# Performance work log

Hardware: AMD Instinct MI355X
Metric: run time of the kernel (lower is better)

The kernel has to match this reference:

```python
import jax, jax.numpy as jnp
import numpy as np
import math

B, S, HID = 1, 2048, 4096
NH, NKV, HD = 32, 8, 128
ROPE_THETA = 500000.0
NEG = -1e9

def _rope_tables(seq_len, head_dim, theta):
    inv_freq = 1.0 / (theta ** (np.arange(0, head_dim, 2, dtype=np.float32) / head_dim))
    t = np.arange(seq_len, dtype=np.float32)
    freqs = np.outer(t, inv_freq)                      # [S, HD/2]
    emb = np.concatenate([freqs, freqs], axis=-1)      # [S, HD]
    return jnp.asarray(np.cos(emb))[None], jnp.asarray(np.sin(emb))[None]  # [1,S,HD]

def setup_inputs() -> dict:
    key = jax.random.key(0)
    ks = jax.random.split(key, 6)
    hidden_states = jax.random.normal(ks[0], (B, S, HID), jnp.float32)
    # causal additive mask [B,1,S,S]
    causal = jnp.triu(jnp.full((S, S), NEG, jnp.float32), k=1)
    attention_mask = jnp.broadcast_to(causal, (B, 1, S, S))
    cos, sin = _rope_tables(S, HD, ROPE_THETA)
    sc = 0.02
    wq = jax.random.normal(ks[1], (NH * HD, HID), jnp.float32) * sc
    wk = jax.random.normal(ks[2], (NKV * HD, HID), jnp.float32) * sc
    wv = jax.random.normal(ks[3], (NKV * HD, HID), jnp.float32) * sc
    wo = jax.random.normal(ks[4], (HID, NH * HD), jnp.float32) * sc
    return {"hidden_states": hidden_states, "attention_mask": attention_mask,
            "cos": cos, "sin": sin, "wq": wq, "wk": wk, "wv": wv, "wo": wo}

def _rotate_half(x):
    x1, x2 = jnp.split(x, 2, axis=-1)
    return jnp.concatenate([-x2, x1], axis=-1)

def reference(hidden_states, attention_mask, cos, sin, wq, wk, wv, wo):
    b, s, _ = hidden_states.shape
    # QKV projections (torch Linear: x @ W^T)
    q = jnp.einsum('bsm,nm->bsn', hidden_states, wq).reshape(b, s, NH, HD).transpose(0, 2, 1, 3)
    k = jnp.einsum('bsm,nm->bsn', hidden_states, wk).reshape(b, s, NKV, HD).transpose(0, 2, 1, 3)
    v = jnp.einsum('bsm,nm->bsn', hidden_states, wv).reshape(b, s, NKV, HD).transpose(0, 2, 1, 3)
    # RoPE (cos/sin broadcast over heads via unsqueeze dim 1)
    c = cos[:, None, :, :]
    sn = sin[:, None, :, :]
    q = q * c + _rotate_half(q) * sn
    k = k * c + _rotate_half(k) * sn
    # GQA: repeat kv heads
    n_rep = NH // NKV
    k = jnp.repeat(k, n_rep, axis=1)
    v = jnp.repeat(v, n_rep, axis=1)
    scores = jnp.einsum('bhqd,bhkd->bhqk', q, k) / math.sqrt(HD)
    scores = scores + attention_mask[:, :, :, :s]
    attn = jax.nn.softmax(scores.astype(jnp.float32), axis=-1).astype(q.dtype)
    out = jnp.einsum('bhqk,bhkd->bhqd', attn, v)        # [b,NH,s,HD]
    out = out.transpose(0, 2, 1, 3).reshape(b, s, NH * HD)
    return jnp.einsum('bsn,mn->bsm', out, wo)
```

## Files before the change

### kernel.cpp

```cpp
#include <hip/hip_runtime.h>
#include <hip/hip_bf16.h>
#include <stdint.h>

typedef __hip_bfloat16 bf16;
using bf16x8 = __attribute__((ext_vector_type(8))) short;
using f32x4  = __attribute__((ext_vector_type(4))) float;

#define MFMA16(a, b, c) __builtin_amdgcn_mfma_f32_16x16x32_bf16(a, b, c, 0, 0, 0)

#define S_LEN 2048
#define HID   4096
#define NH    32
#define NKV   8
#define HD    128
#define DQ    4096
#define DKV   1024
#define QK_SCALE 0.1275228868824805f

__device__ inline void gl_lds16(const bf16* g, bf16* l) {
    __builtin_amdgcn_global_load_lds(
        (const __attribute__((address_space(1))) void*)g,
        (__attribute__((address_space(3))) void*)l, 16, 0, 0);
}

__device__ inline void cvt_store4(const float* src, bf16* dst, size_t i4) {
    float4 v = ((const float4*)src)[i4];
    union { ushort4 u; bf16 h[4]; } pk;
    pk.h[0] = __float2bfloat16(v.x);
    pk.h[1] = __float2bfloat16(v.y);
    pk.h[2] = __float2bfloat16(v.z);
    pk.h[3] = __float2bfloat16(v.w);
    ((ushort4*)dst)[i4] = pk.u;
}

__global__ void conv_all(const float* __restrict__ hidden, const float* __restrict__ wq,
                         const float* __restrict__ wk, const float* __restrict__ wv,
                         bf16* __restrict__ hb, bf16* __restrict__ wqd,
                         bf16* __restrict__ wkd, bf16* __restrict__ wvd) {
    const size_t M1 = 1024 * 1024;
#pragma unroll
    for (int j = 0; j < 4; ++j) {
        size_t idx = (size_t)blockIdx.x * 1024 + j * 256 + threadIdx.x;
        if (idx < 2 * M1)      cvt_store4(hidden, hb,  idx);
        else if (idx < 6 * M1) cvt_store4(wq,     wqd, idx - 2 * M1);
        else if (idx < 7 * M1) cvt_store4(wk,     wkd, idx - 6 * M1);
        else                   cvt_store4(wv,     wvd, idx - 7 * M1);
    }
}

__global__ void conv_wo(const float* __restrict__ wo, bf16* __restrict__ wod) {
#pragma unroll
    for (int j = 0; j < 4; ++j) {
        size_t idx = (size_t)blockIdx.x * 1024 + j * 256 + threadIdx.x;
        cvt_store4(wo, wod, idx);
    }
}

__global__ void __launch_bounds__(256, 2)
qkv_gemm(const bf16* __restrict__ A, const bf16* __restrict__ Bq,
         const bf16* __restrict__ Bk, const bf16* __restrict__ Bv,
         bf16* __restrict__ Cq, bf16* __restrict__ Ck, bf16* __restrict__ Cv) {
    __shared__ __align__(16) bf16 As[128][64];
    __shared__ __align__(16) bf16 Bs[128][64];

    const int bx = blockIdx.x;
    int mode, bn;
    const bf16* B;
    if (bx < 32)      { mode = 0; B = Bq; bn = bx * 128; }
    else if (bx < 40) { mode = 1; B = Bk; bn = (bx - 32) * 128; }
    else              { mode = 2; B = Bv; bn = (bx - 40) * 128; }

    const int tid  = threadIdx.x;
    const int bm   = blockIdx.y * 128;
    const int wave = tid >> 6, lane = tid & 63;
    const int quad = lane >> 4, l15 = lane & 15;
    const int wr   = (wave >> 1) * 64;
    const int wc   = (wave & 1) * 64;

    f32x4 acc[4][4] = {};

    for (int k0 = 0; k0 < HID; k0 += 64) {
#pragma unroll
        for (int i = 0; i < 4; ++i) {
            int idx = tid + i * 256;
            int r   = idx >> 3;
            int c   = (idx & 7) * 8;
            gl_lds16(&A[(size_t)(bm + r) * HID + k0 + c], &As[r][c]);
            gl_lds16(&B[(size_t)(bn + r) * HID + k0 + c], &Bs[r][c]);
        }
        __syncthreads();
#pragma unroll
        for (int kk = 0; kk < 64; kk += 32) {
            bf16x8 a[4], b[4];
#pragma unroll
            for (int i = 0; i < 4; ++i)
                a[i] = *(const bf16x8*)(&As[wr + i * 16 + l15][kk + quad * 8]);
#pragma unroll
            for (int i = 0; i < 4; ++i)
                b[i] = *(const bf16x8*)(&Bs[wc + i * 16 + l15][kk + quad * 8]);
#pragma unroll
            for (int mi = 0; mi < 4; ++mi)
#pragma unroll
                for (int ni = 0; ni < 4; ++ni)
                    acc[mi][ni] = MFMA16(a[mi], b[ni], acc[mi][ni]);
        }
        __syncthreads();
    }

    if (mode == 0) {
#pragma unroll
        for (int mi = 0; mi < 4; ++mi)
#pragma unroll
            for (int ni = 0; ni < 4; ++ni)
#pragma unroll
                for (int r = 0; r < 4; ++r)
                    Cq[(size_t)(bm + wr + mi * 16 + quad * 4 + r) * DQ +
                       bn + wc + ni * 16 + l15] = __float2bfloat16(acc[mi][ni][r]);
    } else if (mode == 1) {
#pragma unroll
        for (int mi = 0; mi < 4; ++mi)
#pragma unroll
            for (int ni = 0; ni < 4; ++ni)
#pragma unroll
                for (int r = 0; r < 4; ++r)
                    Ck[(size_t)(bm + wr + mi * 16 + quad * 4 + r) * DKV +
                       bn + wc + ni * 16 + l15] = __float2bfloat16(acc[mi][ni][r]);
    } else {
#pragma unroll
        for (int mi = 0; mi < 4; ++mi)
#pragma unroll
            for (int ni = 0; ni < 4; ++ni) {
                int row0 = bm + wr + mi * 16 + quad * 4;
                int col  = bn + wc + ni * 16 + l15;
                union { ushort4 u; bf16 h[4]; } pk;
#pragma unroll
                for (int r = 0; r < 4; ++r) pk.h[r] = __float2bfloat16(acc[mi][ni][r]);
                *(ushort4*)(&Cv[(size_t)col * S_LEN + row0]) = pk.u;
            }
    }
}

__global__ void __launch_bounds__(256, 2)
out_gemm(const bf16* __restrict__ A, const bf16* __restrict__ B,
         float* __restrict__ C) {
    __shared__ __align__(16) bf16 As[128][64];
    __shared__ __align__(16) bf16 Bs[128][64];

    const int tid  = threadIdx.x;
    const int bm   = blockIdx.y * 128;
    const int bn   = blockIdx.x * 128;
    const int wave = tid >> 6, lane = tid & 63;
    const int quad = lane >> 4, l15 = lane & 15;
    const int wr   = (wave >> 1) * 64;
    const int wc   = (wave & 1) * 64;

    f32x4 acc[4][4] = {};

    for (int k0 = 0; k0 < DQ; k0 += 64) {
#pragma unroll
        for (int i = 0; i < 4; ++i) {
            int idx = tid + i * 256;
            int r   = idx >> 3;
            int c   = (idx & 7) * 8;
            gl_lds16(&A[(size_t)(bm + r) * DQ + k0 + c], &As[r][c]);
            gl_lds16(&B[(size_t)(bn + r) * DQ + k0 + c], &Bs[r][c]);
        }
        __syncthreads();
#pragma unroll
        for (int kk = 0; kk < 64; kk += 32) {
            bf16x8 a[4], b[4];
#pragma unroll
            for (int i = 0; i < 4; ++i)
                a[i] = *(const bf16x8*)(&As[wr + i * 16 + l15][kk + quad * 8]);
#pragma unroll
            for (int i = 0; i < 4; ++i)
                b[i] = *(const bf16x8*)(&Bs[wc + i * 16 + l15][kk + quad * 8]);
#pragma unroll
            for (int mi = 0; mi < 4; ++mi)
#pragma unroll
                for (int ni = 0; ni < 4; ++ni)
                    acc[mi][ni] = MFMA16(a[mi], b[ni], acc[mi][ni]);
        }
        __syncthreads();
    }

#pragma unroll
    for (int mi = 0; mi < 4; ++mi)
#pragma unroll
        for (int ni = 0; ni < 4; ++ni)
#pragma unroll
            for (int r = 0; r < 4; ++r)
                C[(size_t)(bm + wr + mi * 16 + quad * 4 + r) * HID +
                  bn + wc + ni * 16 + l15] = acc[mi][ni][r];
}

__global__ void rope_all(bf16* __restrict__ q, bf16* __restrict__ k,
                         const float* __restrict__ cosb, const float* __restrict__ sinb) {
    int idx = blockIdx.x * 256 + threadIdx.x;
    const int nq = S_LEN * NH * 64;
    bf16* x;
    int nheads;
    float mul;
    if (idx < nq) { x = q; nheads = NH; mul = QK_SCALE; }
    else          { x = k; nheads = NKV; mul = 1.0f; idx -= nq; }
    int d = idx & 63;
    int h = (idx >> 6) % nheads;
    int s = idx / (nheads * 64);
    size_t base = (size_t)s * nheads * 128 + (size_t)h * 128 + d;
    float x1 = __bfloat162float(x[base]);
    float x2 = __bfloat162float(x[base + 64]);
    x[base]      = __float2bfloat16((x1 * cosb[s * 128 + d]      - x2 * sinb[s * 128 + d])      * mul);
    x[base + 64] = __float2bfloat16((x2 * cosb[s * 128 + d + 64] + x1 * sinb[s * 128 + d + 64]) * mul);
}

__device__ __forceinline__ void stage_kv(const bf16* __restrict__ Kp,
                                         const bf16* __restrict__ Vp,
                                         bf16* ks, bf16* vs, int t0, int tid) {
#pragma unroll
    for (int i = 0; i < 4; ++i) {
        int idx = tid + i * 256;
        int t   = idx >> 4;
        int c8  = ((idx & 15) - t) & 15;
        gl_lds16(&Kp[(size_t)(t0 + t) * DKV + c8 * 8], &ks[idx * 8]);
        int d   = idx >> 3;
        int tc  = ((idx & 7) - d) & 7;
        gl_lds16(&Vp[(size_t)d * S_LEN + t0 + tc * 8], &vs[idx * 8]);
    }
}

__global__ void __launch_bounds__(256, 2)
flash_attn(const bf16* Q, const bf16* __restrict__ K,
           const bf16* __restrict__ Vt, bf16* O) {
    __shared__ __align__(16) bf16 Ks[2][64 * 128];
    __shared__ __align__(16) bf16 Vs[2][128 * 64];
    __shared__ __align__(16) bf16 p_lds[4][16][72];

    const int xb   = (int)gridDim.x - 1 - (int)blockIdx.x;
    const int head = blockIdx.y;
    const int kvh  = head >> 2;
    const int tid  = threadIdx.x;
    const int wave = tid >> 6, lane = tid & 63;
    const int quad = lane >> 4, l15 = lane & 15;
    const int q0w  = xb * 64 + wave * 16;

    const bf16* Kp = K + kvh * HD;
    const bf16* Vp = Vt + (size_t)kvh * HD * S_LEN;

    bf16x8 qf[4];
#pragma unroll
    for (int c = 0; c < 4; ++c)
        qf[c] = *(const bf16x8*)(&Q[(size_t)(q0w + l15) * DQ + head * HD + c * 32 + quad * 8]);

    f32x4 o_acc[8] = {};
    float l_part[4] = {0.f, 0.f, 0.f, 0.f};

    const int t_max = (xb + 1) * 64;

    stage_kv(Kp, Vp, &Ks[0][0], &Vs[0][0], 0, tid);
    asm volatile("s_waitcnt vmcnt(0)" ::: "memory");
    __builtin_amdgcn_sched_barrier(0);
    __builtin_amdgcn_s_barrier();
    __builtin_amdgcn_sched_barrier(0);

    int cur = 0;
    for (int t0 = 0; t0 < t_max; t0 += 64) {
        if (t0 + 64 < t_max)
            stage_kv(Kp, Vp, &Ks[cur ^ 1][0], &Vs[cur ^ 1][0], t0 + 64, tid);
        __builtin_amdgcn_sched_barrier(0);

        const bf16* ksb = &Ks[cur][0];
        const bf16* vsb = &Vs[cur][0];

        f32x4 sc[4] = {};
        __builtin_amdgcn_s_setprio(1);
#pragma unroll
        for (int h = 0; h < 4; ++h) {
            int t = h * 16 + l15;
#pragma unroll
            for (int c = 0; c < 4; ++c) {
                bf16x8 kf = *(const bf16x8*)(&ksb[t * 128 + ((c * 4 + quad + t) & 15) * 8]);
                sc[h] = MFMA16(qf[c], kf, sc[h]);
            }
        }
        __builtin_amdgcn_s_setprio(0);

        if (t0 + 64 > q0w) {
#pragma unroll
            for (int r = 0; r < 4; ++r) {
                const int q = q0w + quad * 4 + r;
                float lsum = 0.f;
#pragma unroll
                for (int h = 0; h < 4; ++h) {
                    float a = (t0 + h * 16 + l15 > q) ? -1e30f : sc[h][r];
                    float p = exp2f(a);
                    lsum += p;
                    p_lds[wave][quad * 4 + r][h * 16 + l15] = __float2bfloat16(p);
                }
                l_part[r] += lsum;
            }
        } else {
#pragma unroll
            for (int r = 0; r < 4; ++r) {
                float lsum = 0.f;
#pragma unroll
                for (int h = 0; h < 4; ++h) {
                    float p = exp2f(sc[h][r]);
                    lsum += p;
                    p_lds[wave][quad * 4 + r][h * 16 + l15] = __float2bfloat16(p);
                }
                l_part[r] += lsum;
            }
        }

        asm volatile("" ::: "memory");
        bf16x8 pf0 = *(const bf16x8*)(&p_lds[wave][l15][quad * 8]);
        bf16x8 pf1 = *(const bf16x8*)(&p_lds[wave][l15][32 + quad * 8]);
        __builtin_amdgcn_s_setprio(1);
#pragma unroll
        for (int db = 0; db < 8; ++db) {
            int d = db * 16 + l15;
            bf16x8 vf0 = *(const bf16x8*)(&vsb[d * 64 + ((quad + d) & 7) * 8]);
            bf16x8 vf1 = *(const bf16x8*)(&vsb[d * 64 + ((4 + quad + d) & 7) * 8]);
            o_acc[db] = MFMA16(pf0, vf0, o_acc[db]);
            o_acc[db] = MFMA16(pf1, vf1, o_acc[db]);
        }
        __builtin_amdgcn_s_setprio(0);

        __builtin_amdgcn_sched_barrier(0);
        asm volatile("s_waitcnt vmcnt(0)" ::: "memory");
        __builtin_amdgcn_sched_barrier(0);
        __builtin_amdgcn_s_barrier();
        __builtin_amdgcn_sched_barrier(0);
        cur ^= 1;
    }

#pragma unroll
    for (int r = 0; r < 4; ++r) {
        float l = l_part[r];
        l += __shfl_xor(l, 1);
        l += __shfl_xor(l, 2);
        l += __shfl_xor(l, 4);
        l += __shfl_xor(l, 8);
        float inv = 1.0f / l;
        int row = q0w + quad * 4 + r;
#pragma unroll
        for (int db = 0; db < 8; ++db)
            O[(size_t)row * DQ + head * HD + db * 16 + l15] =
                __float2bfloat16(o_acc[db][r] * inv);
    }
}

extern "C" void kernel_launch(void* const* d_in, const int* in_sizes, int n_in,
                              void* d_out, int out_size, void* d_ws, size_t ws_size,
                              hipStream_t stream) {
    const float* hidden = (const float*)d_in[0];
    const float* cosb   = (const float*)d_in[2];
    const float* sinb   = (const float*)d_in[3];
    const float* wq     = (const float*)d_in[4];
    const float* wk     = (const float*)d_in[5];
    const float* wv     = (const float*)d_in[6];
    const float* wo     = (const float*)d_in[7];
    float* out = (float*)d_out;

    const size_t M1 = 1024 * 1024;
    bf16* hb  = (bf16*)d_ws;
    bf16* wkd = hb + 8 * M1;
    bf16* wvd = hb + 12 * M1;
    bf16* wod = hb;
    bf16* qb  = hb + 16 * M1;
    bf16* kb  = hb + 24 * M1;
    bf16* vt  = hb + 26 * M1;
    bf16* wqd = (bf16*)d_out;

    conv_all<<<8192, 256, 0, stream>>>(hidden, wq, wk, wv, hb, wqd, wkd, wvd);
    qkv_gemm<<<dim3(48, 16), 256, 0, stream>>>(hb, wqd, wkd, wvd, qb, kb, vt);
    conv_wo<<<4096, 256, 0, stream>>>(wo, wod);
    rope_all<<<(S_LEN * (NH + NKV) * 64) / 256, 256, 0, stream>>>(qb, kb, cosb, sinb);
    flash_attn<<<dim3(32, 32), 256, 0, stream>>>(qb, kb, vt, qb);
    out_gemm<<<dim3(32, 16), 256, 0, stream>>>(qb, wod, out);
}
```

Baseline: 561.1 us.

## Swizzle GEMM LDS tiles, vectorize RoPE, load V directly to registers in attention

Both GEMMs now store A/B tiles in LDS with an XOR-style rotation of 16-byte slots per row, so the MFMA fragment reads avoid bank conflicts. RoPE processes four elements per thread with vector loads of the bf16 data and the cos/sin tables, cutting thread count and scalar memory ops. Flash attention drops the V LDS staging and reads V fragments from global memory straight into registers, which frees LDS so the launch bound can target three blocks per SM. The direct V loads are not double-buffered and may expose global latency and raise register pressure.

```diff
diff --git a/kernel.cpp b/kernel.cpp
--- a/kernel.cpp
+++ b/kernel.cpp
@@ -82,22 +82,27 @@
     for (int k0 = 0; k0 < HID; k0 += 64) {
 #pragma unroll
         for (int i = 0; i < 4; ++i) {
-            int idx = tid + i * 256;
-            int r   = idx >> 3;
-            int c   = (idx & 7) * 8;
-            gl_lds16(&A[(size_t)(bm + r) * HID + k0 + c], &As[r][c]);
-            gl_lds16(&B[(size_t)(bn + r) * HID + k0 + c], &Bs[r][c]);
+            int idx  = tid + i * 256;
+            int r    = idx >> 3;
+            int slot = idx & 7;
+            int c    = ((slot - r) & 7) * 8;
+            gl_lds16(&A[(size_t)(bm + r) * HID + k0 + c], &As[r][slot * 8]);
+            gl_lds16(&B[(size_t)(bn + r) * HID + k0 + c], &Bs[r][slot * 8]);
         }
         __syncthreads();
 #pragma unroll
         for (int kk = 0; kk < 64; kk += 32) {
             bf16x8 a[4], b[4];
 #pragma unroll
-            for (int i = 0; i < 4; ++i)
-                a[i] = *(const bf16x8*)(&As[wr + i * 16 + l15][kk + quad * 8]);
-#pragma unroll
-            for (int i = 0; i < 4; ++i)
-                b[i] = *(const bf16x8*)(&Bs[wc + i * 16 + l15][kk + quad * 8]);
+            for (int i = 0; i < 4; ++i) {
+                int row = wr + i * 16 + l15;
+                a[i] = *(const bf16x8*)(&As[row][(((kk >> 3) + quad + row) & 7) * 8]);
+            }
+#pragma unroll
+            for (int i = 0; i < 4; ++i) {
+                int row = wc + i * 16 + l15;
+                b[i] = *(const bf16x8*)(&Bs[row][(((kk >> 3) + quad + row) & 7) * 8]);
+            }
 #pragma unroll
             for (int mi = 0; mi < 4; ++mi)
 #pragma unroll
@@ -159,22 +164,27 @@
     for (int k0 = 0; k0 < DQ; k0 += 64) {
 #pragma unroll
         for (int i = 0; i < 4; ++i) {
-            int idx = tid + i * 256;
-            int r   = idx >> 3;
-            int c   = (idx & 7) * 8;
-            gl_lds16(&A[(size_t)(bm + r) * DQ + k0 + c], &As[r][c]);
-            gl_lds16(&B[(size_t)(bn + r) * DQ + k0 + c], &Bs[r][c]);
+            int idx  = tid + i * 256;
+            int r    = idx >> 3;
+            int slot = idx & 7;
+            int c    = ((slot - r) & 7) * 8;
+            gl_lds16(&A[(size_t)(bm + r) * DQ + k0 + c], &As[r][slot * 8]);
+            gl_lds16(&B[(size_t)(bn + r) * DQ + k0 + c], &Bs[r][slot * 8]);
         }
         __syncthreads();
 #pragma unroll
         for (int kk = 0; kk < 64; kk += 32) {
             bf16x8 a[4], b[4];
 #pragma unroll
-            for (int i = 0; i < 4; ++i)
-                a[i] = *(const bf16x8*)(&As[wr + i * 16 + l15][kk + quad * 8]);
-#pragma unroll
-            for (int i = 0; i < 4; ++i)
-                b[i] = *(const bf16x8*)(&Bs[wc + i * 16 + l15][kk + quad * 8]);
+            for (int i = 0; i < 4; ++i) {
+                int row = wr + i * 16 + l15;
+                a[i] = *(const bf16x8*)(&As[row][(((kk >> 3) + quad + row) & 7) * 8]);
+            }
+#pragma unroll
+            for (int i = 0; i < 4; ++i) {
+                int row = wc + i * 16 + l15;
+                b[i] = *(const bf16x8*)(&Bs[row][(((kk >> 3) + quad + row) & 7) * 8]);
+            }
 #pragma unroll
             for (int mi = 0; mi < 4; ++mi)
 #pragma unroll
@@ -197,42 +207,51 @@
 __global__ void rope_all(bf16* __restrict__ q, bf16* __restrict__ k,
                          const float* __restrict__ cosb, const float* __restrict__ sinb) {
     int idx = blockIdx.x * 256 + threadIdx.x;
-    const int nq = S_LEN * NH * 64;
+    const int nq = S_LEN * NH * 16;
     bf16* x;
     int nheads;
     float mul;
     if (idx < nq) { x = q; nheads = NH; mul = QK_SCALE; }
     else          { x = k; nheads = NKV; mul = 1.0f; idx -= nq; }
-    int d = idx & 63;
-    int h = (idx >> 6) % nheads;
-    int s = idx / (nheads * 64);
-    size_t base = (size_t)s * nheads * 128 + (size_t)h * 128 + d;
-    float x1 = __bfloat162float(x[base]);
-    float x2 = __bfloat162float(x[base + 64]);
-    x[base]      = __float2bfloat16((x1 * cosb[s * 128 + d]      - x2 * sinb[s * 128 + d])      * mul);
-    x[base + 64] = __float2bfloat16((x2 * cosb[s * 128 + d + 64] + x1 * sinb[s * 128 + d + 64]) * mul);
-}
-
-__device__ __forceinline__ void stage_kv(const bf16* __restrict__ Kp,
-                                         const bf16* __restrict__ Vp,
-                                         bf16* ks, bf16* vs, int t0, int tid) {
+    int d4 = (idx & 15) * 4;
+    int h  = (idx >> 4) % nheads;
+    int s  = idx / (nheads * 16);
+    size_t base = (size_t)s * nheads * 128 + (size_t)h * 128 + d4;
+    union { ushort4 u; bf16 hh[4]; } i1, i2, o1, o2;
+    i1.u = *(const ushort4*)(&x[base]);
+    i2.u = *(const ushort4*)(&x[base + 64]);
+    float4 c1 = *(const float4*)(&cosb[s * 128 + d4]);
+    float4 c2 = *(const float4*)(&cosb[s * 128 + d4 + 64]);
+    float4 s1 = *(const float4*)(&sinb[s * 128 + d4]);
+    float4 s2 = *(const float4*)(&sinb[s * 128 + d4 + 64]);
+#pragma unroll
+    for (int j = 0; j < 4; ++j) {
+        float x1 = __bfloat162float(i1.hh[j]);
+        float x2 = __bfloat162float(i2.hh[j]);
+        float cc1 = ((const float*)&c1)[j], cc2 = ((const float*)&c2)[j];
+        float ss1 = ((const float*)&s1)[j], ss2 = ((const float*)&s2)[j];
+        o1.hh[j] = __float2bfloat16((x1 * cc1 - x2 * ss1) * mul);
+        o2.hh[j] = __float2bfloat16((x2 * cc2 + x1 * ss2) * mul);
+    }
+    *(ushort4*)(&x[base])      = o1.u;
+    *(ushort4*)(&x[base + 64]) = o2.u;
+}
+
+__device__ __forceinline__ void stage_k(const bf16* __restrict__ Kp,
+                                        bf16* ks, int t0, int tid) {
 #pragma unroll
     for (int i = 0; i < 4; ++i) {
         int idx = tid + i * 256;
         int t   = idx >> 4;
         int c8  = ((idx & 15) - t) & 15;
         gl_lds16(&Kp[(size_t)(t0 + t) * DKV + c8 * 8], &ks[idx * 8]);
-        int d   = idx >> 3;
-        int tc  = ((idx & 7) - d) & 7;
-        gl_lds16(&Vp[(size_t)d * S_LEN + t0 + tc * 8], &vs[idx * 8]);
-    }
-}
-
-__global__ void __launch_bounds__(256, 2)
+    }
+}
+
+__global__ void __launch_bounds__(256, 3)
 flash_attn(const bf16* Q, const bf16* __restrict__ K,
            const bf16* __restrict__ Vt, bf16* O) {
     __shared__ __align__(16) bf16 Ks[2][64 * 128];
-    __shared__ __align__(16) bf16 Vs[2][128 * 64];
     __shared__ __align__(16) bf16 p_lds[4][16][72];
 
     const int xb   = (int)gridDim.x - 1 - (int)blockIdx.x;
@@ -256,7 +275,7 @@
 
     const int t_max = (xb + 1) * 64;
 
-    stage_kv(Kp, Vp, &Ks[0][0], &Vs[0][0], 0, tid);
+    stage_k(Kp, &Ks[0][0], 0, tid);
     asm volatile("s_waitcnt vmcnt(0)" ::: "memory");
     __builtin_amdgcn_sched_barrier(0);
     __builtin_amdgcn_s_barrier();
@@ -264,12 +283,18 @@
 
     int cur = 0;
     for (int t0 = 0; t0 < t_max; t0 += 64) {
+        bf16x8 va0[4], va1[4];
+#pragma unroll
+        for (int db = 0; db < 4; ++db) {
+            const bf16* vb = &Vp[(size_t)(db * 16 + l15) * S_LEN + t0 + quad * 8];
+            va0[db] = *(const bf16x8*)(vb);
+            va1[db] = *(const bf16x8*)(vb + 32);
+        }
         if (t0 + 64 < t_max)
-            stage_kv(Kp, Vp, &Ks[cur ^ 1][0], &Vs[cur ^ 1][0], t0 + 64, tid);
+            stage_k(Kp, &Ks[cur ^ 1][0], t0 + 64, tid);
         __builtin_amdgcn_sched_barrier(0);
 
         const bf16* ksb = &Ks[cur][0];
-        const bf16* vsb = &Vs[cur][0];
 
         f32x4 sc[4] = {};
         __builtin_amdgcn_s_setprio(1);
@@ -283,6 +308,14 @@
             }
         }
         __builtin_amdgcn_s_setprio(0);
+
+        bf16x8 vb0[4], vb1[4];
+#pragma unroll
+        for (int db = 0; db < 4; ++db) {
+            const bf16* vb = &Vp[(size_t)((db + 4) * 16 + l15) * S_LEN + t0 + quad * 8];
+            vb0[db] = *(const bf16x8*)(vb);
+            vb1[db] = *(const bf16x8*)(vb + 32);
+        }
 
         if (t0 + 64 > q0w) {
 #pragma unroll
@@ -317,12 +350,14 @@
         bf16x8 pf1 = *(const bf16x8*)(&p_lds[wave][l15][32 + quad * 8]);
         __builtin_amdgcn_s_setprio(1);
 #pragma unroll
-        for (int db = 0; db < 8; ++db) {
-            int d = db * 16 + l15;
-            bf16x8 vf0 = *(const bf16x8*)(&vsb[d * 64 + ((quad + d) & 7) * 8]);
-            bf16x8 vf1 = *(const bf16x8*)(&vsb[d * 64 + ((4 + quad + d) & 7) * 8]);
-            o_acc[db] = MFMA16(pf0, vf0, o_acc[db]);
-            o_acc[db] = MFMA16(pf1, vf1, o_acc[db]);
+        for (int db = 0; db < 4; ++db) {
+            o_acc[db] = MFMA16(pf0, va0[db], o_acc[db]);
+            o_acc[db] = MFMA16(pf1, va1[db], o_acc[db]);
+        }
+#pragma unroll
+        for (int db = 0; db < 4; ++db) {
+            o_acc[db + 4] = MFMA16(pf0, vb0[db], o_acc[db + 4]);
+            o_acc[db + 4] = MFMA16(pf1, vb1[db], o_acc[db + 4]);
         }
         __builtin_amdgcn_s_setprio(0);
 
@@ -375,7 +410,7 @@
     conv_all<<<8192, 256, 0, stream>>>(hidden, wq, wk, wv, hb, wqd, wkd, wvd);
     qkv_gemm<<<dim3(48, 16), 256, 0, stream>>>(hb, wqd, wkd, wvd, qb, kb, vt);
     conv_wo<<<4096, 256, 0, stream>>>(wo, wod);
-    rope_all<<<(S_LEN * (NH + NKV) * 64) / 256, 256, 0, stream>>>(qb, kb, cosb, sinb);
+    rope_all<<<(S_LEN * (NH + NKV) * 16) / 256, 256, 0, stream>>>(qb, kb, cosb, sinb);
     flash_attn<<<dim3(32, 32), 256, 0, stream>>>(qb, kb, vt, qb);
     out_gemm<<<dim3(32, 16), 256, 0, stream>>>(qb, wod, out);
 }
```

New measurement: 803.6 us. 1.43x slower.
